# Performance work log

Measured on AMD Instinct MI355X. Metric: run time of the kernel, lower is better.

Reference implementation:

```python
import jax, jax.numpy as jnp
import numpy as np

KH = KW = 3
STRIDE = 1
PAD = 1
K_CHUNK = 16  # chunk size along the C*kh*kw patch dim to bound the [N,F,kc,L] intermediate


def _unfold(x):
    # Mirrors torch.nn.functional.unfold: output [N, C*KH*KW, Ho*Wo], c-major then (kh, kw).
    N, C, H, W = x.shape
    Ho = (H - KH + 2 * PAD) // STRIDE + 1
    Wo = (W - KW + 2 * PAD) // STRIDE + 1
    xp = jnp.pad(x, ((0, 0), (0, 0), (PAD, PAD), (PAD, PAD)))
    pats = jnp.stack(
        [xp[:, :, i:i + STRIDE * Ho:STRIDE, j:j + STRIDE * Wo:STRIDE]
         for i in range(KH) for j in range(KW)],
        axis=2,
    )  # [N, C, KH*KW, Ho, Wo]
    return pats.reshape(N, C * KH * KW, Ho * Wo), Ho, Wo


def _chunk_dist(xc, wc):
    # xc: [N, kc, L], wc: [F, kc] -> partial L1 sums over this K-chunk: [N, F, L]
    return jnp.abs(xc[:, None, :, :] - wc[None, :, :, None]).sum(axis=2)


def _adder2d(x, W):
    # out[n, f, i, j] = -sum_k |Xcol[n, k, l] - Wcol[f, k]|  (AdderNet L1 'correlation')
    N = x.shape[0]
    F = W.shape[0]
    Xcol, Ho, Wo = _unfold(x)          # [N, K, L]
    Wcol = W.reshape(F, -1)            # [F, K]
    K = Wcol.shape[1]
    chunk = jax.checkpoint(_chunk_dist)  # remat so backward never stores [N,F,K,L] signs
    acc = jnp.zeros((N, F, Ho * Wo), x.dtype)
    for s in range(0, K, K_CHUNK):     # fixed structural loop over patch dim (K=288 -> 18 chunks)
        acc = acc + chunk(Xcol[:, s:s + K_CHUNK, :], Wcol[:, s:s + K_CHUNK])
    return -acc.reshape(N, F, Ho, Wo)


def setup_inputs() -> dict:
    key = jax.random.key(0)
    kx, kw = jax.random.split(key)
    x = jax.random.normal(kx, (16, 32, 56, 56), dtype=jnp.float32)
    # kaiming_normal_ scale on [64,32,3,3]: std = sqrt(2 / fan_in), fan_in = 32*3*3
    W = jax.random.normal(kw, (64, 32, 3, 3), dtype=jnp.float32) * np.sqrt(2.0 / (32 * 3 * 3)).astype(np.float32)
    return {"x": x, "W": W}


def reference(x, W):
    return _adder2d(x, W)
```

## Files before the change

kernel.cpp:

```cpp
#include <hip/hip_runtime.h>


#define N_    16
#define C_    32
#define H_    56
#define F_    64
#define KDIM  288
#define CCH   16
#define NCH   (C_/CCH)
#define ROWS  2
#define XROWS (ROWS+2)
#define XSTR  58
#define SPT   7
#define FPT   4
#define TPB   256

__global__ __launch_bounds__(TPB, 2)
void adder2d_kernel(const float* __restrict__ x,
                    const float* __restrict__ w,
                    float* __restrict__ out) {
    __shared__ float xs[CCH][XROWS][XSTR];
    __shared__ float wt[CCH * 9][F_];

    const int tid = threadIdx.x;
    const int bid = blockIdx.x;
    const int n   = bid / 28;
    const int rt  = bid % 28;
    const int i0  = rt * ROWS;

    const int fg = tid >> 4;
    const int sg = tid & 15;
    const int ir = sg >> 3;
    const int j0 = (sg & 7) * SPT;
    const int f0 = fg * FPT;

    float acc[FPT][SPT];
    #pragma unroll
    for (int f = 0; f < FPT; ++f)
        #pragma unroll
        for (int s = 0; s < SPT; ++s) acc[f][s] = 0.0f;

    for (int ch = 0; ch < NCH; ++ch) {
        const int c0 = ch * CCH;
        __syncthreads();

        for (int e = tid; e < CCH * XROWS * XSTR; e += TPB) {
            const int c  = e / (XROWS * XSTR);
            const int r  = (e / XSTR) % XROWS;
            const int cp = e % XSTR;
            const int rp = i0 + r;
            float v = 0.0f;
            if (rp >= 1 && rp <= H_ && cp >= 1 && cp <= H_)
                v = x[((n * C_ + c0 + c) * H_ + (rp - 1)) * H_ + (cp - 1)];
            xs[c][r][cp] = v;
        }
        for (int e = tid; e < CCH * 9 * F_; e += TPB) {
            const int kk = e >> 6;
            const int f  = e & 63;
            wt[kk][f] = w[f * KDIM + c0 * 9 + kk];
        }
        __syncthreads();

        for (int c = 0; c < CCH; ++c) {
            #pragma unroll
            for (int kh = 0; kh < 3; ++kh) {
                float xw[SPT + 2];
                #pragma unroll
                for (int t = 0; t < SPT + 2; ++t)
                    xw[t] = xs[c][ir + kh][j0 + t];
                #pragma unroll
                for (int kw = 0; kw < 3; ++kw) {
                    const float4 wv = *(const float4*)&wt[c * 9 + kh * 3 + kw][f0];
                    const float wf[FPT] = {wv.x, wv.y, wv.z, wv.w};
                    #pragma unroll
                    for (int f = 0; f < FPT; ++f)
                        #pragma unroll
                        for (int s = 0; s < SPT; ++s)
                            acc[f][s] += fabsf(xw[s + kw] - wf[f]);
                }
            }
        }
    }

    const int orow = i0 + ir;
    #pragma unroll
    for (int f = 0; f < FPT; ++f) {
        float* op = &out[((n * F_ + f0 + f) * H_ + orow) * H_ + j0];
        #pragma unroll
        for (int s = 0; s < SPT; ++s) op[s] = -acc[f][s];
    }
}

extern "C" void kernel_launch(void* const* d_in, const int* in_sizes, int n_in,
                              void* d_out, int out_size, void* d_ws, size_t ws_size,
                              hipStream_t stream) {
    const float* x = (const float*)d_in[0];
    const float* w = (const float*)d_in[1];
    float* out = (float*)d_out;
    adder2d_kernel<<<dim3(N_ * 28), dim3(TPB), 0, stream>>>(x, w, out);
}
```

Measured before the change: 90.41 us.

## Replace LDS-tiled kernel with wave-per-8x8-tile kernel reading x and padded weights directly

Replaces the shared-memory tiled kernel with a 64-thread block per 8x8 output tile and 8-filter group. Each lane computes one pixel across 8 filters and reads its 3x3 input window straight from global memory, using precomputed offsets and masks. A separate prep kernel pads the weights to 12 per filter in a workspace so they can be loaded as uniform, vectorizable loads. This removes LDS staging and barriers but gives up register blocking across pixels: each input value now feeds only 8 filters, so load traffic per FLOP rises and the second launch adds overhead.

```diff
diff --git a/kernel.cpp b/kernel.cpp
--- a/kernel.cpp
+++ b/kernel.cpp
@@ -1,94 +1,82 @@
 #include <hip/hip_runtime.h>
 
 
-#define N_    16
-#define C_    32
-#define H_    56
-#define F_    64
-#define KDIM  288
-#define CCH   16
-#define NCH   (C_/CCH)
-#define ROWS  2
-#define XROWS (ROWS+2)
-#define XSTR  58
-#define SPT   7
-#define FPT   4
-#define TPB   256
+#define H_   56
+#define C_   32
+#define F_   64
+#define N_   16
+#define HW_  (H_ * H_)
+#define FPW  8
+#define NFG  (F_ / FPW)
+#define NT   49
+#define WPAD_ELTS (C_ * F_ * 12)
 
-__global__ __launch_bounds__(TPB, 2)
-void adder2d_kernel(const float* __restrict__ x,
-                    const float* __restrict__ w,
-                    float* __restrict__ out) {
-    __shared__ float xs[CCH][XROWS][XSTR];
-    __shared__ float wt[CCH * 9][F_];
+__global__ __launch_bounds__(64)
+void prep_w(const float* __restrict__ w, float* __restrict__ wpad) {
+    int idx = blockIdx.x * 64 + threadIdx.x;
+    if (idx >= WPAD_ELTS) return;
+    int c   = idx / (F_ * 12);
+    int rem = idx % (F_ * 12);
+    int f   = rem / 12;
+    int kk  = rem % 12;
+    wpad[idx] = (kk < 9) ? w[f * (C_ * 9) + c * 9 + kk] : 0.0f;
+}
 
-    const int tid = threadIdx.x;
+__global__ __launch_bounds__(64)
+void adder_main(const float* __restrict__ x,
+                const float* __restrict__ wpad,
+                float* __restrict__ out) {
+    const int lane = threadIdx.x;
+    const int lr = lane >> 3;
+    const int lc = lane & 7;
     const int bid = blockIdx.x;
-    const int n   = bid / 28;
-    const int rt  = bid % 28;
-    const int i0  = rt * ROWS;
+    const int fg = bid & (NFG - 1);
+    const int t  = (bid >> 3) % NT;
+    const int n  = bid / (NT * NFG);
+    const int r0 = (t / 7) * 8;
+    const int c0 = (t % 7) * 8;
+    const int f0 = fg * FPW;
 
-    const int fg = tid >> 4;
-    const int sg = tid & 15;
-    const int ir = sg >> 3;
-    const int j0 = (sg & 7) * SPT;
-    const int f0 = fg * FPT;
-
-    float acc[FPT][SPT];
+    int   off[9];
+    float msk[9];
     #pragma unroll
-    for (int f = 0; f < FPT; ++f)
+    for (int kh = 0; kh < 3; ++kh) {
         #pragma unroll
-        for (int s = 0; s < SPT; ++s) acc[f][s] = 0.0f;
-
-    for (int ch = 0; ch < NCH; ++ch) {
-        const int c0 = ch * CCH;
-        __syncthreads();
-
-        for (int e = tid; e < CCH * XROWS * XSTR; e += TPB) {
-            const int c  = e / (XROWS * XSTR);
-            const int r  = (e / XSTR) % XROWS;
-            const int cp = e % XSTR;
-            const int rp = i0 + r;
-            float v = 0.0f;
-            if (rp >= 1 && rp <= H_ && cp >= 1 && cp <= H_)
-                v = x[((n * C_ + c0 + c) * H_ + (rp - 1)) * H_ + (cp - 1)];
-            xs[c][r][cp] = v;
-        }
-        for (int e = tid; e < CCH * 9 * F_; e += TPB) {
-            const int kk = e >> 6;
-            const int f  = e & 63;
-            wt[kk][f] = w[f * KDIM + c0 * 9 + kk];
-        }
-        __syncthreads();
-
-        for (int c = 0; c < CCH; ++c) {
-            #pragma unroll
-            for (int kh = 0; kh < 3; ++kh) {
-                float xw[SPT + 2];
-                #pragma unroll
-                for (int t = 0; t < SPT + 2; ++t)
-                    xw[t] = xs[c][ir + kh][j0 + t];
-                #pragma unroll
-                for (int kw = 0; kw < 3; ++kw) {
-                    const float4 wv = *(const float4*)&wt[c * 9 + kh * 3 + kw][f0];
-                    const float wf[FPT] = {wv.x, wv.y, wv.z, wv.w};
-                    #pragma unroll
-                    for (int f = 0; f < FPT; ++f)
-                        #pragma unroll
-                        for (int s = 0; s < SPT; ++s)
-                            acc[f][s] += fabsf(xw[s + kw] - wf[f]);
-                }
-            }
+        for (int kw = 0; kw < 3; ++kw) {
+            int rp = r0 + lr + kh - 1;
+            int cp = c0 + lc + kw - 1;
+            bool v = (rp >= 0 && rp < H_ && cp >= 0 && cp < H_);
+            off[kh * 3 + kw] = v ? rp * H_ + cp : 0;
+            msk[kh * 3 + kw] = v ? 1.0f : 0.0f;
         }
     }
 
-    const int orow = i0 + ir;
+    float acc[FPW];
     #pragma unroll
-    for (int f = 0; f < FPT; ++f) {
-        float* op = &out[((n * F_ + f0 + f) * H_ + orow) * H_ + j0];
+    for (int f = 0; f < FPW; ++f) acc[f] = 0.0f;
+
+    const float* xb = x + n * C_ * HW_;
+
+    #pragma unroll 2
+    for (int c = 0; c < C_; ++c) {
+        float xv[9];
         #pragma unroll
-        for (int s = 0; s < SPT; ++s) op[s] = -acc[f][s];
+        for (int k = 0; k < 9; ++k)
+            xv[k] = xb[c * HW_ + off[k]] * msk[k];
+
+        const float* wp = wpad + (c * F_ + f0) * 12;
+        #pragma unroll
+        for (int f = 0; f < FPW; ++f) {
+            #pragma unroll
+            for (int k = 0; k < 9; ++k)
+                acc[f] += fabsf(xv[k] - wp[f * 12 + k]);
+        }
     }
+
+    const int orow = r0 + lr, ocol = c0 + lc;
+    #pragma unroll
+    for (int f = 0; f < FPW; ++f)
+        out[((n * F_ + f0 + f) * H_ + orow) * H_ + ocol] = -acc[f];
 }
 
 extern "C" void kernel_launch(void* const* d_in, const int* in_sizes, int n_in,
@@ -96,6 +84,9 @@
                               hipStream_t stream) {
     const float* x = (const float*)d_in[0];
     const float* w = (const float*)d_in[1];
-    float* out = (float*)d_out;
-    adder2d_kernel<<<dim3(N_ * 28), dim3(TPB), 0, stream>>>(x, w, out);
+    float* out  = (float*)d_out;
+    float* wpad = (float*)d_ws;
+
+    prep_w<<<dim3((WPAD_ELTS + 63) / 64), dim3(64), 0, stream>>>(w, wpad);
+    adder_main<<<dim3(N_ * NT * NFG), dim3(64), 0, stream>>>(x, wpad, out);
 }
```

New measurement: 94.75 us. 4.8% more time.
